# Optimization experiments

Measured on AMD Instinct MI355X. Metric: run time of the kernel, lower is better.

The kernel has to match this reference:

```python
import jax, jax.numpy as jnp
import numpy as np

GROUPS = [[0, 1, 2, 3, 4], [5, 7, 9], [6, 8, 10], [11, 13, 15], [12, 14, 16]]
G = len(GROUPS)
BN_EPS = 1e-5


def _fc_edges(n):
    r = np.repeat(np.arange(n), n)
    c = np.tile(np.arange(n), n)
    m = r != c
    return jnp.asarray(r[m]), jnp.asarray(c[m])


ROW, COL = _fc_edges(G)  # [E], E = G*(G-1) = 20


def _bn(x, scale, bias, mean, var):
    # inference-mode batchnorm over last dim
    return (x - mean) * (scale * jax.lax.rsqrt(var + BN_EPS)) + bias


def setup_inputs() -> dict:
    key = jax.random.key(0)
    ks = jax.random.split(key, 12)
    B, K, C, Ci = 4096, 17, 256, 64
    inp = {
        "x_bk_c": jax.random.normal(ks[0], (B * K, C), jnp.float32),
        "W_down": jax.random.normal(ks[1], (C, Ci), jnp.float32) * 0.05,
        "b_down": jax.random.normal(ks[2], (Ci,), jnp.float32) * 0.05,
        "bn1_scale": jax.random.uniform(ks[3], (Ci,), jnp.float32, 0.5, 1.5),
        "bn1_bias": jax.random.normal(ks[4], (Ci,), jnp.float32) * 0.1,
        "bn1_mean": jax.random.normal(ks[5], (Ci,), jnp.float32) * 0.1,
        "bn1_var": jax.random.uniform(ks[6], (Ci,), jnp.float32, 0.5, 1.5),
        "W_conv": jax.random.normal(ks[7], (Ci, 2 * Ci), jnp.float32) * 0.05,  # 1x1 conv, bias=False
        "bn2_scale": jax.random.uniform(ks[8], (Ci,), jnp.float32, 0.5, 1.5),
        "bn2_bias": jax.random.normal(ks[9], (Ci,), jnp.float32) * 0.1,
        "bn2_mean": jax.random.normal(ks[10], (Ci,), jnp.float32) * 0.1,
        "bn2_var": jax.random.uniform(ks[11], (Ci,), jnp.float32, 0.5, 1.5),
        "W_agg": jax.random.normal(jax.random.fold_in(key, 100), (Ci, C), jnp.float32) * 0.05,
        "b_agg": jax.random.normal(jax.random.fold_in(key, 101), (C,), jnp.float32) * 0.05,
        "B": B,
        "K": K,
    }
    return inp


def reference(x_bk_c, W_down, b_down, bn1_scale, bn1_bias, bn1_mean, bn1_var,
              W_conv, bn2_scale, bn2_bias, bn2_mean, bn2_var, W_agg, b_agg, B, K):
    C = x_bk_c.shape[-1]
    # down-projection + BN + SiLU
    xd = jax.nn.silu(_bn(x_bk_c @ W_down + b_down, bn1_scale, bn1_bias, bn1_mean, bn1_var))
    xd = xd.reshape(B, K, -1)  # [B, K, Ci]
    # per-group mean pooling (static small loop over 5 groups)
    means = jnp.stack([xd[:, g, :].mean(axis=1) for g in GROUPS], axis=1)  # [B, G, Ci]
    # EdgeConv over fully-connected group graph
    x_i = means[:, ROW, :]                                   # [B, E, Ci]
    x_j = means[:, COL, :]
    ef = jnp.concatenate([x_i, x_j - x_i], axis=-1)          # [B, E, 2Ci]
    pe = jax.nn.silu(_bn(ef @ W_conv.T, bn2_scale, bn2_bias, bn2_mean, bn2_var))  # [B, E, Ci]
    agg = jnp.zeros_like(means).at[:, ROW, :].add(pe)        # scatter-add over target nodes
    # per-group attention scores in C_in
    att = jax.nn.sigmoid(agg @ W_agg + b_agg)                # [B, G, C]
    # average group scores over each keypoint's memberships
    M = np.zeros((K, G), np.float32)
    for gi, g in enumerate(GROUPS):
        for kp in g:
            M[kp, gi] += 1.0
    Mj = jnp.asarray(M)
    cnt = Mj.sum(axis=1, keepdims=True)                      # [K, 1]
    ssum = jnp.einsum('kg,bgc->bkc', Mj, att)                # [B, K, C]
    safe = jnp.where(cnt > 0, cnt, 1.0)
    final = jnp.where(cnt > 0, ssum / safe, 1.0)             # ungrouped kps -> 1.0
    return (x_bk_c.reshape(B, K, C) * final).reshape(B * K, C)
```

## Files before the change

kernel.cpp:

```cpp
#include <hip/hip_runtime.h>

typedef float  v4f    __attribute__((ext_vector_type(4)));
typedef float  f32x4  __attribute__((ext_vector_type(4)));
typedef short  bf16x8 __attribute__((ext_vector_type(8)));
typedef short  bf16x4 __attribute__((ext_vector_type(4)));

namespace {
constexpr int XBSTR = 264;
constexpr int XDT   = 24;
constexpr int MWC   = 129;
constexpr int ATS   = 260;
constexpr int MSTR  = 72;
constexpr int FRAG_SLOTS = 5120;

__device__ __forceinline__ float fsilu(float v){ return v/(1.f+__expf(-v)); }
__device__ __forceinline__ float fsigm(float v){ return 1.f/(1.f+__expf(-v)); }

__device__ __forceinline__ unsigned f2bf2(float a, float b){
  unsigned r;
  asm("v_cvt_pk_bf16_f32 %0, %1, %2" : "=v"(r) : "v"(a), "v"(b));
  return r;
}
__device__ __forceinline__ short f2bf(float f){
  unsigned u = __builtin_bit_cast(unsigned, f);
  return (short)((u + 0x7FFFu + ((u>>16)&1u)) >> 16);
}
__device__ __forceinline__ float bf2f(short s){
  unsigned u = ((unsigned)(unsigned short)s) << 16;
  return __builtin_bit_cast(float, u);
}

template<bool USE_WS>
__device__ __forceinline__ bf16x8 get_bd(const bf16x8* wsf, const float* Wd,
                                         int nt, int ks, int l){
  if constexpr (USE_WS) return wsf[(nt*8 + ks)*64 + l];
  bf16x8 f;
  #pragma unroll
  for (int j = 0; j < 8; ++j) f[j] = f2bf(Wd[(ks*32 + (l>>4)*8 + j)*64 + nt*16 + (l&15)]);
  return f;
}
template<bool USE_WS>
__device__ __forceinline__ bf16x8 get_bc(const bf16x8* wsf, const float* Wc,
                                         int nt, int ks, int l){
  if constexpr (USE_WS) return wsf[2048 + (nt*2 + ks)*64 + l];
  const int col = nt*16 + (l&15), cw = col>>6, co = col&63;
  bf16x8 f;
  #pragma unroll
  for (int j = 0; j < 8; ++j) f[j] = f2bf(Wc[co*128 + cw*64 + ks*32 + (l>>4)*8 + j]);
  return f;
}
template<bool USE_WS>
__device__ __forceinline__ bf16x8 get_ba(const bf16x8* wsf, const float* Wa,
                                         int nt, int ks, int l){
  if constexpr (USE_WS) return wsf[3072 + (nt*2 + ks)*64 + l];
  const int col = nt*16 + (l&15);
  bf16x8 f;
  #pragma unroll
  for (int j = 0; j < 8; ++j) f[j] = f2bf(Wa[(ks*32 + (l>>4)*8 + j)*256 + col]);
  return f;
}
}

__global__ __launch_bounds__(256)
void pack_frags(const float* __restrict__ Wd, const float* __restrict__ Wc,
                const float* __restrict__ Wa, bf16x8* __restrict__ wsf)
{
  const int e  = blockIdx.x*256 + threadIdx.x;
  const int l  = e & 63;
  const int fi = e >> 6;
  bf16x8 f;
  if (fi < 32) {
    const int nt = fi >> 3, ks = fi & 7;
    #pragma unroll
    for (int j = 0; j < 8; ++j) f[j] = f2bf(Wd[(ks*32 + (l>>4)*8 + j)*64 + nt*16 + (l&15)]);
  } else if (fi < 48) {
    const int idx = fi - 32, nt = idx >> 1, ks = idx & 1;
    const int col = nt*16 + (l&15), cw = col>>6, co = col&63;
    #pragma unroll
    for (int j = 0; j < 8; ++j) f[j] = f2bf(Wc[co*128 + cw*64 + ks*32 + (l>>4)*8 + j]);
  } else {
    const int idx = fi - 48, nt = idx >> 1, ks = idx & 1;
    const int col = nt*16 + (l&15);
    #pragma unroll
    for (int j = 0; j < 8; ++j) f[j] = f2bf(Wa[(ks*32 + (l>>4)*8 + j)*256 + col]);
  }
  wsf[e] = f;
}

template<bool USE_WS>
__global__ __launch_bounds__(256, 5)
void fused_gnn_v12(const float* __restrict__ x,
                   const float* __restrict__ Wd, const float* __restrict__ bd,
                   const float* __restrict__ bn1s, const float* __restrict__ bn1b,
                   const float* __restrict__ bn1m, const float* __restrict__ bn1v,
                   const float* __restrict__ Wc,
                   const float* __restrict__ bn2s, const float* __restrict__ bn2b,
                   const float* __restrict__ bn2m, const float* __restrict__ bn2v,
                   const float* __restrict__ Wa, const float* __restrict__ ba,
                   const bf16x8* __restrict__ wsf,
                   float* __restrict__ out)
{
  __shared__ short xbf[18*XBSTR];
  __shared__ __align__(16) char uni_raw[3072];
  __shared__ float mw[5*MWC];
  __shared__ short mbf[16*MSTR];
  __shared__ short abf[16*MSTR];

  short* xdT = (short*)uni_raw;
  short* att = (short*)uni_raw;

  const int tid  = threadIdx.x;
  const int l    = tid & 63;
  const int wv   = tid >> 6;
  const int arow = l & 15;
  const int ak8  = (l >> 4) * 8;
  const int b    = blockIdx.x;
  const int colA = wv*16 + arow;

  const float a1r = bn1s[colA] * rsqrtf(bn1v[colA] + 1e-5f);
  const float b1r = (bd[colA] - bn1m[colA])*a1r + bn1b[colA];
  const float a2r = bn2s[l] * rsqrtf(bn2v[l] + 1e-5f);
  const float b2r = bn2b[l] - bn2m[l]*a2r;

  const int c4 = l*4;
  const int r0 = tid >> 6;
  v4f xr0, xr1, xr2, xr3, xr4;
  {
    const v4f* x4 = (const v4f*)(x + (size_t)b * 4352);
    xr0 = x4[tid];        xr1 = x4[256 + tid];
    xr2 = x4[512 + tid];  xr3 = x4[768 + tid];
    if (tid < 64) xr4 = x4[1024 + tid];
    auto store4 = [&](v4f v, int r){
      uint2 u; u.x = f2bf2(v.x, v.y); u.y = f2bf2(v.z, v.w);
      *(uint2*)&xbf[r*XBSTR + c4] = u;
    };
    store4(xr0, r0);      store4(xr1, r0 + 4);
    store4(xr2, r0 + 8);  store4(xr3, r0 + 12);
    if (tid < 64) store4(xr4, 16);
  }
  __syncthreads();

  {
    f32x4 acc0 = {0.f,0.f,0.f,0.f};
    f32x4 acc1 = {0.f,0.f,0.f,0.f};
    const int rowT = (arow == 0) ? 16 : 17;
    #pragma unroll
    for (int h = 0; h < 2; ++h) {
      bf16x8 Bd[4];
      #pragma unroll
      for (int k4 = 0; k4 < 4; ++k4) Bd[k4] = get_bd<USE_WS>(wsf, Wd, wv, h*4 + k4, l);
      #pragma unroll
      for (int k4 = 0; k4 < 4; ++k4) {
        const int ks = h*4 + k4;
        bf16x8 a0 = *(const bf16x8*)&xbf[arow*XBSTR + ks*32 + ak8];
        acc0 = __builtin_amdgcn_mfma_f32_16x16x32_bf16(a0, Bd[k4], acc0, 0, 0, 0);
        bf16x8 a1 = *(const bf16x8*)&xbf[rowT*XBSTR + ks*32 + ak8];
        acc1 = __builtin_amdgcn_mfma_f32_16x16x32_bf16(a1, Bd[k4], acc1, 0, 0, 0);
      }
    }
    const float s0 = fsilu(acc0[0]*a1r + b1r);
    const float s1 = fsilu(acc0[1]*a1r + b1r);
    const float s2 = fsilu(acc0[2]*a1r + b1r);
    const float s3 = fsilu(acc0[3]*a1r + b1r);
    uint2 u; u.x = f2bf2(s0, s1); u.y = f2bf2(s2, s3);
    *(uint2*)&xdT[colA*XDT + (l>>4)*4] = u;
    if ((l >> 4) == 0)
      xdT[colA*XDT + 16] = f2bf(fsilu(acc1[0]*a1r + b1r));
  }
  __syncthreads();

  bf16x8 BcT[2][2];
  #pragma unroll
  for (int t = 0; t < 2; ++t)
    #pragma unroll
    for (int ks = 0; ks < 2; ++ks)
      BcT[t][ks] = get_bc<USE_WS>(wsf, Wc, wv*2 + t, ks, l);

  {
    const int i = l;
    #define XDV(r) bf2f(xdT[i*XDT + (r)])
    if (wv == 0) {
      mbf[0*MSTR + i] = f2bf((XDV(0)+XDV(1)+XDV(2)+XDV(3)+XDV(4))*0.2f);
      mbf[4*MSTR + i] = f2bf((XDV(12)+XDV(14)+XDV(16))*(1.f/3.f));
    } else if (wv == 1) {
      mbf[1*MSTR + i] = f2bf((XDV(5)+XDV(7)+XDV(9))*(1.f/3.f));
    } else if (wv == 2) {
      mbf[2*MSTR + i] = f2bf((XDV(6)+XDV(8)+XDV(10))*(1.f/3.f));
    } else {
      mbf[3*MSTR + i] = f2bf((XDV(11)+XDV(13)+XDV(15))*(1.f/3.f));
    }
    #undef XDV
  }
  __syncthreads();

  {
    bf16x8 am[2];
    #pragma unroll
    for (int ks = 0; ks < 2; ++ks)
      am[ks] = *(const bf16x8*)&mbf[arow*MSTR + ks*32 + ak8];
    #pragma unroll
    for (int t = 0; t < 2; ++t) {
      const int nt = wv*2 + t;
      f32x4 acc = {0.f,0.f,0.f,0.f};
      #pragma unroll
      for (int ks = 0; ks < 2; ++ks)
        acc = __builtin_amdgcn_mfma_f32_16x16x32_bf16(am[ks], BcT[t][ks], acc, 0, 0, 0);
      if ((l >> 4) == 0) {
        #pragma unroll
        for (int j = 0; j < 4; ++j) mw[j*MWC + nt*16 + arow] = acc[j];
      } else if ((l >> 4) == 1) {
        mw[4*MWC + nt*16 + arow] = acc[0];
      }
    }
  }
  __syncthreads();

  bf16x8 BaT[4][2];
  #pragma unroll
  for (int t = 0; t < 4; ++t)
    #pragma unroll
    for (int ks = 0; ks < 2; ++ks)
      BaT[t][ks] = get_ba<USE_WS>(wsf, Wa, wv*4 + t, ks, l);

  {
    const int o = l;
    float m2c[5];
    #pragma unroll
    for (int cc = 0; cc < 5; ++cc) m2c[cc] = mw[cc*MWC + 64 + o];
    auto doG = [&](int g){
      const float bse = mw[g*MWC + o] - m2c[g];
      float s = 0.f;
      #pragma unroll
      for (int cc = 0; cc < 5; ++cc) {
        if (cc != g) s += fsilu((bse + m2c[cc])*a2r + b2r);
      }
      abf[g*MSTR + o] = f2bf(s);
    };
    if (wv == 0) { doG(0); doG(4); }
    else if (wv == 1) doG(1);
    else if (wv == 2) doG(2);
    else doG(3);
  }
  __syncthreads();

  {
    bf16x8 ae[2];
    #pragma unroll
    for (int ks = 0; ks < 2; ++ks)
      ae[ks] = *(const bf16x8*)&abf[arow*MSTR + ks*32 + ak8];
    #pragma unroll
    for (int t = 0; t < 4; ++t) {
      const int nt = wv*4 + t;
      const int colE = nt*16 + arow;
      f32x4 acc = {0.f,0.f,0.f,0.f};
      #pragma unroll
      for (int ks = 0; ks < 2; ++ks)
        acc = __builtin_amdgcn_mfma_f32_16x16x32_bf16(ae[ks], BaT[t][ks], acc, 0, 0, 0);
      const float bav = ba[colE];
      const int q4 = l >> 4;
      if (q4 == 0) {
        #pragma unroll
        for (int j = 0; j < 4; ++j)
          att[j*ATS + colE] = f2bf(fsigm(acc[j] + bav));
      } else if (q4 == 1) {
        att[4*ATS + colE] = f2bf(fsigm(acc[0] + bav));
      }
    }
  }
  __syncthreads();

  {
    float* og = out + (size_t)b*4352;
    constexpr int GOF[17] = {0,0,0,0,0,1,2,1,2,1,2,3,4,3,4,3,4};
    auto emit = [&](v4f xv, int k){
      const bf16x4 a4 = *(const bf16x4*)&att[GOF[k]*ATS + c4];
      v4f o;
      o.x = xv.x * bf2f(a4[0]);
      o.y = xv.y * bf2f(a4[1]);
      o.z = xv.z * bf2f(a4[2]);
      o.w = xv.w * bf2f(a4[3]);
      *(v4f*)&og[k*256 + c4] = o;
    };
    emit(xr0, r0);      emit(xr1, r0 + 4);
    emit(xr2, r0 + 8);  emit(xr3, r0 + 12);
    if (tid < 64) emit(xr4, 16);
  }
}

extern "C" void kernel_launch(void* const* d_in, const int* in_sizes, int n_in,
                              void* d_out, int out_size, void* d_ws, size_t ws_size,
                              hipStream_t stream) {
    (void)n_in; (void)out_size;
    const float* x   = (const float*)d_in[0];
    const float* Wd  = (const float*)d_in[1];
    const float* bd  = (const float*)d_in[2];
    const float* s1  = (const float*)d_in[3];
    const float* b1  = (const float*)d_in[4];
    const float* m1  = (const float*)d_in[5];
    const float* v1  = (const float*)d_in[6];
    const float* Wc  = (const float*)d_in[7];
    const float* s2  = (const float*)d_in[8];
    const float* b2  = (const float*)d_in[9];
    const float* m2  = (const float*)d_in[10];
    const float* v2  = (const float*)d_in[11];
    const float* Wa  = (const float*)d_in[12];
    const float* ba  = (const float*)d_in[13];

    const int Btot = in_sizes[0] / (17 * 256);
    bf16x8* wsf = (bf16x8*)d_ws;

    if (ws_size >= (size_t)FRAG_SLOTS * 16) {
        pack_frags<<<FRAG_SLOTS/256, 256, 0, stream>>>(Wd, Wc, Wa, wsf);
        fused_gnn_v12<true><<<Btot, 256, 0, stream>>>(
            x, Wd, bd, s1, b1, m1, v1, Wc, s2, b2, m2, v2, Wa, ba,
            wsf, (float*)d_out);
    } else {
        fused_gnn_v12<false><<<Btot, 256, 0, stream>>>(
            x, Wd, bd, s1, b1, m1, v1, Wc, s2, b2, m2, v2, Wa, ba,
            wsf, (float*)d_out);
    }
}
```

Baseline: 41.52 us.

## Process two batch items per block with prefetched second input tile

```diff
diff --git a/kernel.cpp b/kernel.cpp
--- a/kernel.cpp
+++ b/kernel.cpp
@@ -88,8 +88,8 @@
 }
 
 template<bool USE_WS>
-__global__ __launch_bounds__(256, 5)
-void fused_gnn_v12(const float* __restrict__ x,
+__global__ __launch_bounds__(256, 7)
+void fused_gnn_v13(const float* __restrict__ x,
                    const float* __restrict__ Wd, const float* __restrict__ bd,
                    const float* __restrict__ bn1s, const float* __restrict__ bn1b,
                    const float* __restrict__ bn1m, const float* __restrict__ bn1v,
@@ -114,176 +114,193 @@
   const int wv   = tid >> 6;
   const int arow = l & 15;
   const int ak8  = (l >> 4) * 8;
-  const int b    = blockIdx.x;
+  const int b0   = blockIdx.x * 2;
   const int colA = wv*16 + arow;
+  const int c4   = l*4;
+  const int r0   = tid >> 6;
 
   const float a1r = bn1s[colA] * rsqrtf(bn1v[colA] + 1e-5f);
   const float b1r = (bd[colA] - bn1m[colA])*a1r + bn1b[colA];
   const float a2r = bn2s[l] * rsqrtf(bn2v[l] + 1e-5f);
   const float b2r = bn2b[l] - bn2m[l]*a2r;
 
-  const int c4 = l*4;
-  const int r0 = tid >> 6;
-  v4f xr0, xr1, xr2, xr3, xr4;
+  auto store4 = [&](v4f v, int r){
+    uint2 u; u.x = f2bf2(v.x, v.y); u.y = f2bf2(v.z, v.w);
+    *(uint2*)&xbf[r*XBSTR + c4] = u;
+  };
+
+  v4f xr[2][5];
   {
-    const v4f* x4 = (const v4f*)(x + (size_t)b * 4352);
-    xr0 = x4[tid];        xr1 = x4[256 + tid];
-    xr2 = x4[512 + tid];  xr3 = x4[768 + tid];
-    if (tid < 64) xr4 = x4[1024 + tid];
-    auto store4 = [&](v4f v, int r){
-      uint2 u; u.x = f2bf2(v.x, v.y); u.y = f2bf2(v.z, v.w);
-      *(uint2*)&xbf[r*XBSTR + c4] = u;
-    };
-    store4(xr0, r0);      store4(xr1, r0 + 4);
-    store4(xr2, r0 + 8);  store4(xr3, r0 + 12);
-    if (tid < 64) store4(xr4, 16);
+    const v4f* x4 = (const v4f*)(x + (size_t)b0 * 4352);
+    #pragma unroll
+    for (int i = 0; i < 4; ++i) xr[0][i] = x4[i*256 + tid];
+    if (tid < 64) xr[0][4] = x4[1024 + tid];
+    store4(xr[0][0], r0);      store4(xr[0][1], r0 + 4);
+    store4(xr[0][2], r0 + 8);  store4(xr[0][3], r0 + 12);
+    if (tid < 64) store4(xr[0][4], 16);
+    const v4f* y4 = x4 + 1088;
+    #pragma unroll
+    for (int i = 0; i < 4; ++i) xr[1][i] = y4[i*256 + tid];
+    if (tid < 64) xr[1][4] = y4[1024 + tid];
   }
   __syncthreads();
 
-  {
-    f32x4 acc0 = {0.f,0.f,0.f,0.f};
-    f32x4 acc1 = {0.f,0.f,0.f,0.f};
-    const int rowT = (arow == 0) ? 16 : 17;
-    #pragma unroll
-    for (int h = 0; h < 2; ++h) {
-      bf16x8 Bd[4];
-      #pragma unroll
-      for (int k4 = 0; k4 < 4; ++k4) Bd[k4] = get_bd<USE_WS>(wsf, Wd, wv, h*4 + k4, l);
-      #pragma unroll
-      for (int k4 = 0; k4 < 4; ++k4) {
-        const int ks = h*4 + k4;
-        bf16x8 a0 = *(const bf16x8*)&xbf[arow*XBSTR + ks*32 + ak8];
-        acc0 = __builtin_amdgcn_mfma_f32_16x16x32_bf16(a0, Bd[k4], acc0, 0, 0, 0);
-        bf16x8 a1 = *(const bf16x8*)&xbf[rowT*XBSTR + ks*32 + ak8];
-        acc1 = __builtin_amdgcn_mfma_f32_16x16x32_bf16(a1, Bd[k4], acc1, 0, 0, 0);
+  #pragma unroll
+  for (int it = 0; it < 2; ++it) {
+    const int b = b0 + it;
+
+    {
+      f32x4 acc0 = {0.f,0.f,0.f,0.f};
+      f32x4 acc1 = {0.f,0.f,0.f,0.f};
+      const int rowT = (arow == 0) ? 16 : 17;
+      #pragma unroll
+      for (int h = 0; h < 2; ++h) {
+        bf16x8 Bd[4];
+        #pragma unroll
+        for (int k4 = 0; k4 < 4; ++k4) Bd[k4] = get_bd<USE_WS>(wsf, Wd, wv, h*4 + k4, l);
+        #pragma unroll
+        for (int k4 = 0; k4 < 4; ++k4) {
+          const int ks = h*4 + k4;
+          bf16x8 a0 = *(const bf16x8*)&xbf[arow*XBSTR + ks*32 + ak8];
+          acc0 = __builtin_amdgcn_mfma_f32_16x16x32_bf16(a0, Bd[k4], acc0, 0, 0, 0);
+          bf16x8 a1 = *(const bf16x8*)&xbf[rowT*XBSTR + ks*32 + ak8];
+          acc1 = __builtin_amdgcn_mfma_f32_16x16x32_bf16(a1, Bd[k4], acc1, 0, 0, 0);
+        }
       }
-    }
-    const float s0 = fsilu(acc0[0]*a1r + b1r);
-    const float s1 = fsilu(acc0[1]*a1r + b1r);
-    const float s2 = fsilu(acc0[2]*a1r + b1r);
-    const float s3 = fsilu(acc0[3]*a1r + b1r);
-    uint2 u; u.x = f2bf2(s0, s1); u.y = f2bf2(s2, s3);
-    *(uint2*)&xdT[colA*XDT + (l>>4)*4] = u;
-    if ((l >> 4) == 0)
-      xdT[colA*XDT + 16] = f2bf(fsilu(acc1[0]*a1r + b1r));
-  }
-  __syncthreads();
-
-  bf16x8 BcT[2][2];
-  #pragma unroll
-  for (int t = 0; t < 2; ++t)
-    #pragma unroll
-    for (int ks = 0; ks < 2; ++ks)
-      BcT[t][ks] = get_bc<USE_WS>(wsf, Wc, wv*2 + t, ks, l);
-
-  {
-    const int i = l;
-    #define XDV(r) bf2f(xdT[i*XDT + (r)])
-    if (wv == 0) {
-      mbf[0*MSTR + i] = f2bf((XDV(0)+XDV(1)+XDV(2)+XDV(3)+XDV(4))*0.2f);
-      mbf[4*MSTR + i] = f2bf((XDV(12)+XDV(14)+XDV(16))*(1.f/3.f));
-    } else if (wv == 1) {
-      mbf[1*MSTR + i] = f2bf((XDV(5)+XDV(7)+XDV(9))*(1.f/3.f));
-    } else if (wv == 2) {
-      mbf[2*MSTR + i] = f2bf((XDV(6)+XDV(8)+XDV(10))*(1.f/3.f));
-    } else {
-      mbf[3*MSTR + i] = f2bf((XDV(11)+XDV(13)+XDV(15))*(1.f/3.f));
-    }
-    #undef XDV
-  }
-  __syncthreads();
-
-  {
-    bf16x8 am[2];
-    #pragma unroll
-    for (int ks = 0; ks < 2; ++ks)
-      am[ks] = *(const bf16x8*)&mbf[arow*MSTR + ks*32 + ak8];
-    #pragma unroll
-    for (int t = 0; t < 2; ++t) {
-      const int nt = wv*2 + t;
-      f32x4 acc = {0.f,0.f,0.f,0.f};
+      const float s0 = fsilu(acc0[0]*a1r + b1r);
+      const float s1 = fsilu(acc0[1]*a1r + b1r);
+      const float s2 = fsilu(acc0[2]*a1r + b1r);
+      const float s3 = fsilu(acc0[3]*a1r + b1r);
+      uint2 u; u.x = f2bf2(s0, s1); u.y = f2bf2(s2, s3);
+      *(uint2*)&xdT[colA*XDT + (l>>4)*4] = u;
+      if ((l >> 4) == 0)
+        xdT[colA*XDT + 16] = f2bf(fsilu(acc1[0]*a1r + b1r));
+    }
+    __syncthreads();
+
+    if (it == 0) {
+      store4(xr[1][0], r0);      store4(xr[1][1], r0 + 4);
+      store4(xr[1][2], r0 + 8);  store4(xr[1][3], r0 + 12);
+      if (tid < 64) store4(xr[1][4], 16);
+    }
+
+    bf16x8 BcT[2][2];
+    #pragma unroll
+    for (int t = 0; t < 2; ++t)
       #pragma unroll
       for (int ks = 0; ks < 2; ++ks)
-        acc = __builtin_amdgcn_mfma_f32_16x16x32_bf16(am[ks], BcT[t][ks], acc, 0, 0, 0);
-      if ((l >> 4) == 0) {
-        #pragma unroll
-        for (int j = 0; j < 4; ++j) mw[j*MWC + nt*16 + arow] = acc[j];
-      } else if ((l >> 4) == 1) {
-        mw[4*MWC + nt*16 + arow] = acc[0];
+        BcT[t][ks] = get_bc<USE_WS>(wsf, Wc, wv*2 + t, ks, l);
+
+    {
+      const int i = l;
+      #define XDV(r) bf2f(xdT[i*XDT + (r)])
+      if (wv == 0) {
+        mbf[0*MSTR + i] = f2bf((XDV(0)+XDV(1)+XDV(2)+XDV(3)+XDV(4))*0.2f);
+        mbf[4*MSTR + i] = f2bf((XDV(12)+XDV(14)+XDV(16))*(1.f/3.f));
+      } else if (wv == 1) {
+        mbf[1*MSTR + i] = f2bf((XDV(5)+XDV(7)+XDV(9))*(1.f/3.f));
+      } else if (wv == 2) {
+        mbf[2*MSTR + i] = f2bf((XDV(6)+XDV(8)+XDV(10))*(1.f/3.f));
+      } else {
+        mbf[3*MSTR + i] = f2bf((XDV(11)+XDV(13)+XDV(15))*(1.f/3.f));
       }
-    }
-  }
-  __syncthreads();
-
-  bf16x8 BaT[4][2];
-  #pragma unroll
-  for (int t = 0; t < 4; ++t)
-    #pragma unroll
-    for (int ks = 0; ks < 2; ++ks)
-      BaT[t][ks] = get_ba<USE_WS>(wsf, Wa, wv*4 + t, ks, l);
-
-  {
-    const int o = l;
-    float m2c[5];
-    #pragma unroll
-    for (int cc = 0; cc < 5; ++cc) m2c[cc] = mw[cc*MWC + 64 + o];
-    auto doG = [&](int g){
-      const float bse = mw[g*MWC + o] - m2c[g];
-      float s = 0.f;
-      #pragma unroll
-      for (int cc = 0; cc < 5; ++cc) {
-        if (cc != g) s += fsilu((bse + m2c[cc])*a2r + b2r);
+      #undef XDV
+    }
+    __syncthreads();
+
+    {
+      bf16x8 am[2];
+      #pragma unroll
+      for (int ks = 0; ks < 2; ++ks)
+        am[ks] = *(const bf16x8*)&mbf[arow*MSTR + ks*32 + ak8];
+      #pragma unroll
+      for (int t = 0; t < 2; ++t) {
+        const int nt = wv*2 + t;
+        f32x4 acc = {0.f,0.f,0.f,0.f};
+        #pragma unroll
+        for (int ks = 0; ks < 2; ++ks)
+          acc = __builtin_amdgcn_mfma_f32_16x16x32_bf16(am[ks], BcT[t][ks], acc, 0, 0, 0);
+        if ((l >> 4) == 0) {
+          #pragma unroll
+          for (int j = 0; j < 4; ++j) mw[j*MWC + nt*16 + arow] = acc[j];
+        } else if ((l >> 4) == 1) {
+          mw[4*MWC + nt*16 + arow] = acc[0];
+        }
       }
-      abf[g*MSTR + o] = f2bf(s);
-    };
-    if (wv == 0) { doG(0); doG(4); }
-    else if (wv == 1) doG(1);
-    else if (wv == 2) doG(2);
-    else doG(3);
-  }
-  __syncthreads();
-
-  {
-    bf16x8 ae[2];
-    #pragma unroll
-    for (int ks = 0; ks < 2; ++ks)
-      ae[ks] = *(const bf16x8*)&abf[arow*MSTR + ks*32 + ak8];
-    #pragma unroll
-    for (int t = 0; t < 4; ++t) {
-      const int nt = wv*4 + t;
-      const int colE = nt*16 + arow;
-      f32x4 acc = {0.f,0.f,0.f,0.f};
+    }
+    __syncthreads();
+
+    bf16x8 BaT[4][2];
+    #pragma unroll
+    for (int t = 0; t < 4; ++t)
       #pragma unroll
       for (int ks = 0; ks < 2; ++ks)
-        acc = __builtin_amdgcn_mfma_f32_16x16x32_bf16(ae[ks], BaT[t][ks], acc, 0, 0, 0);
-      const float bav = ba[colE];
-      const int q4 = l >> 4;
-      if (q4 == 0) {
-        #pragma unroll
-        for (int j = 0; j < 4; ++j)
-          att[j*ATS + colE] = f2bf(fsigm(acc[j] + bav));
-      } else if (q4 == 1) {
-        att[4*ATS + colE] = f2bf(fsigm(acc[0] + bav));
+        BaT[t][ks] = get_ba<USE_WS>(wsf, Wa, wv*4 + t, ks, l);
+
+    {
+      const int o = l;
+      float m2c[5];
+      #pragma unroll
+      for (int cc = 0; cc < 5; ++cc) m2c[cc] = mw[cc*MWC + 64 + o];
+      auto doG = [&](int g){
+        const float bse = mw[g*MWC + o] - m2c[g];
+        float s = 0.f;
+        #pragma unroll
+        for (int cc = 0; cc < 5; ++cc) {
+          if (cc != g) s += fsilu((bse + m2c[cc])*a2r + b2r);
+        }
+        abf[g*MSTR + o] = f2bf(s);
+      };
+      if (wv == 0) { doG(0); doG(4); }
+      else if (wv == 1) doG(1);
+      else if (wv == 2) doG(2);
+      else doG(3);
+    }
+    __syncthreads();
+
+    {
+      bf16x8 ae[2];
+      #pragma unroll
+      for (int ks = 0; ks < 2; ++ks)
+        ae[ks] = *(const bf16x8*)&abf[arow*MSTR + ks*32 + ak8];
+      #pragma unroll
+      for (int t = 0; t < 4; ++t) {
+        const int nt = wv*4 + t;
+        const int colE = nt*16 + arow;
+        f32x4 acc = {0.f,0.f,0.f,0.f};
+        #pragma unroll
+        for (int ks = 0; ks < 2; ++ks)
+          acc = __builtin_amdgcn_mfma_f32_16x16x32_bf16(ae[ks], BaT[t][ks], acc, 0, 0, 0);
+        const float bav = ba[colE];
+        const int q4 = l >> 4;
+        if (q4 == 0) {
+          #pragma unroll
+          for (int j = 0; j < 4; ++j)
+            att[j*ATS + colE] = f2bf(fsigm(acc[j] + bav));
+        } else if (q4 == 1) {
+          att[4*ATS + colE] = f2bf(fsigm(acc[0] + bav));
+        }
       }
     }
-  }
-  __syncthreads();
-
-  {
-    float* og = out + (size_t)b*4352;
-    constexpr int GOF[17] = {0,0,0,0,0,1,2,1,2,1,2,3,4,3,4,3,4};
-    auto emit = [&](v4f xv, int k){
-      const bf16x4 a4 = *(const bf16x4*)&att[GOF[k]*ATS + c4];
-      v4f o;
-      o.x = xv.x * bf2f(a4[0]);
-      o.y = xv.y * bf2f(a4[1]);
-      o.z = xv.z * bf2f(a4[2]);
-      o.w = xv.w * bf2f(a4[3]);
-      *(v4f*)&og[k*256 + c4] = o;
-    };
-    emit(xr0, r0);      emit(xr1, r0 + 4);
-    emit(xr2, r0 + 8);  emit(xr3, r0 + 12);
-    if (tid < 64) emit(xr4, 16);
+    __syncthreads();
+
+    {
+      float* og = out + (size_t)b*4352;
+      constexpr int GOF[17] = {0,0,0,0,0,1,2,1,2,1,2,3,4,3,4,3,4};
+      auto emit = [&](v4f xv, int k){
+        const bf16x4 a4 = *(const bf16x4*)&att[GOF[k]*ATS + c4];
+        v4f o;
+        o.x = xv.x * bf2f(a4[0]);
+        o.y = xv.y * bf2f(a4[1]);
+        o.z = xv.z * bf2f(a4[2]);
+        o.w = xv.w * bf2f(a4[3]);
+        *(v4f*)&og[k*256 + c4] = o;
+      };
+      emit(xr[it][0], r0);      emit(xr[it][1], r0 + 4);
+      emit(xr[it][2], r0 + 8);  emit(xr[it][3], r0 + 12);
+      if (tid < 64) emit(xr[it][4], 16);
+    }
+    if (it == 0) __syncthreads();
   }
 }
 
@@ -307,15 +324,16 @@
     const float* ba  = (const float*)d_in[13];
 
     const int Btot = in_sizes[0] / (17 * 256);
+    const int GRID = Btot / 2;
     bf16x8* wsf = (bf16x8*)d_ws;
 
     if (ws_size >= (size_t)FRAG_SLOTS * 16) {
         pack_frags<<<FRAG_SLOTS/256, 256, 0, stream>>>(Wd, Wc, Wa, wsf);
-        fused_gnn_v12<true><<<Btot, 256, 0, stream>>>(
+        fused_gnn_v13<true><<<GRID, 256, 0, stream>>>(
             x, Wd, bd, s1, b1, m1, v1, Wc, s2, b2, m2, v2, Wa, ba,
             wsf, (float*)d_out);
     } else {
-        fused_gnn_v12<false><<<Btot, 256, 0, stream>>>(
+        fused_gnn_v13<false><<<GRID, 256, 0, stream>>>(
             x, Wd, bd, s1, b1, m1, v1, Wc, s2, b2, m2, v2, Wa, ba,
             wsf, (float*)d_out);
     }
```

Result: slower. 139.7 us (+236.5%).

## Process two batch items per block and prefetch the second item's input

Applied to the files above, without the earlier changes.

```diff
diff --git a/kernel.cpp b/kernel.cpp
--- a/kernel.cpp
+++ b/kernel.cpp
@@ -89,7 +89,7 @@
 
 template<bool USE_WS>
 __global__ __launch_bounds__(256, 5)
-void fused_gnn_v12(const float* __restrict__ x,
+void fused_gnn_v14(const float* __restrict__ x,
                    const float* __restrict__ Wd, const float* __restrict__ bd,
                    const float* __restrict__ bn1s, const float* __restrict__ bn1b,
                    const float* __restrict__ bn1m, const float* __restrict__ bn1v,
@@ -114,48 +114,39 @@
   const int wv   = tid >> 6;
   const int arow = l & 15;
   const int ak8  = (l >> 4) * 8;
-  const int b    = blockIdx.x;
+  const int b0   = blockIdx.x * 2;
   const int colA = wv*16 + arow;
+  const int c4   = l*4;
+  const int r0   = tid >> 6;
 
   const float a1r = bn1s[colA] * rsqrtf(bn1v[colA] + 1e-5f);
   const float b1r = (bd[colA] - bn1m[colA])*a1r + bn1b[colA];
   const float a2r = bn2s[l] * rsqrtf(bn2v[l] + 1e-5f);
   const float b2r = bn2b[l] - bn2m[l]*a2r;
 
-  const int c4 = l*4;
-  const int r0 = tid >> 6;
-  v4f xr0, xr1, xr2, xr3, xr4;
-  {
-    const v4f* x4 = (const v4f*)(x + (size_t)b * 4352);
-    xr0 = x4[tid];        xr1 = x4[256 + tid];
-    xr2 = x4[512 + tid];  xr3 = x4[768 + tid];
-    if (tid < 64) xr4 = x4[1024 + tid];
-    auto store4 = [&](v4f v, int r){
-      uint2 u; u.x = f2bf2(v.x, v.y); u.y = f2bf2(v.z, v.w);
-      *(uint2*)&xbf[r*XBSTR + c4] = u;
-    };
-    store4(xr0, r0);      store4(xr1, r0 + 4);
-    store4(xr2, r0 + 8);  store4(xr3, r0 + 12);
-    if (tid < 64) store4(xr4, 16);
-  }
-  __syncthreads();
-
-  {
+  auto store4 = [&](v4f v, int r){
+    uint2 u; u.x = f2bf2(v.x, v.y); u.y = f2bf2(v.z, v.w);
+    *(uint2*)&xbf[r*XBSTR + c4] = u;
+  };
+
+  auto phaseA = [&](){
     f32x4 acc0 = {0.f,0.f,0.f,0.f};
     f32x4 acc1 = {0.f,0.f,0.f,0.f};
     const int rowT = (arow == 0) ? 16 : 17;
     #pragma unroll
     for (int h = 0; h < 2; ++h) {
-      bf16x8 Bd[4];
-      #pragma unroll
-      for (int k4 = 0; k4 < 4; ++k4) Bd[k4] = get_bd<USE_WS>(wsf, Wd, wv, h*4 + k4, l);
+      bf16x8 Bd0 = get_bd<USE_WS>(wsf, Wd, wv, h*4 + 0, l);
+      bf16x8 Bd1 = get_bd<USE_WS>(wsf, Wd, wv, h*4 + 1, l);
+      bf16x8 Bd2 = get_bd<USE_WS>(wsf, Wd, wv, h*4 + 2, l);
+      bf16x8 Bd3 = get_bd<USE_WS>(wsf, Wd, wv, h*4 + 3, l);
       #pragma unroll
       for (int k4 = 0; k4 < 4; ++k4) {
         const int ks = h*4 + k4;
+        const bf16x8 Bd = (k4==0)?Bd0:(k4==1)?Bd1:(k4==2)?Bd2:Bd3;
         bf16x8 a0 = *(const bf16x8*)&xbf[arow*XBSTR + ks*32 + ak8];
-        acc0 = __builtin_amdgcn_mfma_f32_16x16x32_bf16(a0, Bd[k4], acc0, 0, 0, 0);
+        acc0 = __builtin_amdgcn_mfma_f32_16x16x32_bf16(a0, Bd, acc0, 0, 0, 0);
         bf16x8 a1 = *(const bf16x8*)&xbf[rowT*XBSTR + ks*32 + ak8];
-        acc1 = __builtin_amdgcn_mfma_f32_16x16x32_bf16(a1, Bd[k4], acc1, 0, 0, 0);
+        acc1 = __builtin_amdgcn_mfma_f32_16x16x32_bf16(a1, Bd, acc1, 0, 0, 0);
       }
     }
     const float s0 = fsilu(acc0[0]*a1r + b1r);
@@ -166,17 +157,9 @@
     *(uint2*)&xdT[colA*XDT + (l>>4)*4] = u;
     if ((l >> 4) == 0)
       xdT[colA*XDT + 16] = f2bf(fsilu(acc1[0]*a1r + b1r));
-  }
-  __syncthreads();
-
-  bf16x8 BcT[2][2];
-  #pragma unroll
-  for (int t = 0; t < 2; ++t)
-    #pragma unroll
-    for (int ks = 0; ks < 2; ++ks)
-      BcT[t][ks] = get_bc<USE_WS>(wsf, Wc, wv*2 + t, ks, l);
-
-  {
+  };
+
+  auto phaseB1 = [&](){
     const int i = l;
     #define XDV(r) bf2f(xdT[i*XDT + (r)])
     if (wv == 0) {
@@ -190,21 +173,17 @@
       mbf[3*MSTR + i] = f2bf((XDV(11)+XDV(13)+XDV(15))*(1.f/3.f));
     }
     #undef XDV
-  }
-  __syncthreads();
-
-  {
-    bf16x8 am[2];
-    #pragma unroll
-    for (int ks = 0; ks < 2; ++ks)
-      am[ks] = *(const bf16x8*)&mbf[arow*MSTR + ks*32 + ak8];
+  };
+
+  auto phaseB2 = [&](){
+    bf16x8 am0 = *(const bf16x8*)&mbf[arow*MSTR + 0*32 + ak8];
+    bf16x8 am1 = *(const bf16x8*)&mbf[arow*MSTR + 1*32 + ak8];
     #pragma unroll
     for (int t = 0; t < 2; ++t) {
       const int nt = wv*2 + t;
       f32x4 acc = {0.f,0.f,0.f,0.f};
-      #pragma unroll
-      for (int ks = 0; ks < 2; ++ks)
-        acc = __builtin_amdgcn_mfma_f32_16x16x32_bf16(am[ks], BcT[t][ks], acc, 0, 0, 0);
+      acc = __builtin_amdgcn_mfma_f32_16x16x32_bf16(am0, get_bc<USE_WS>(wsf, Wc, nt, 0, l), acc, 0, 0, 0);
+      acc = __builtin_amdgcn_mfma_f32_16x16x32_bf16(am1, get_bc<USE_WS>(wsf, Wc, nt, 1, l), acc, 0, 0, 0);
       if ((l >> 4) == 0) {
         #pragma unroll
         for (int j = 0; j < 4; ++j) mw[j*MWC + nt*16 + arow] = acc[j];
@@ -212,50 +191,39 @@
         mw[4*MWC + nt*16 + arow] = acc[0];
       }
     }
-  }
-  __syncthreads();
-
-  bf16x8 BaT[4][2];
-  #pragma unroll
-  for (int t = 0; t < 4; ++t)
-    #pragma unroll
-    for (int ks = 0; ks < 2; ++ks)
-      BaT[t][ks] = get_ba<USE_WS>(wsf, Wa, wv*4 + t, ks, l);
-
-  {
+  };
+
+  auto phaseB3 = [&](){
     const int o = l;
-    float m2c[5];
-    #pragma unroll
-    for (int cc = 0; cc < 5; ++cc) m2c[cc] = mw[cc*MWC + 64 + o];
-    auto doG = [&](int g){
-      const float bse = mw[g*MWC + o] - m2c[g];
+    float m2c0 = mw[0*MWC + 64 + o], m2c1 = mw[1*MWC + 64 + o];
+    float m2c2 = mw[2*MWC + 64 + o], m2c3 = mw[3*MWC + 64 + o];
+    float m2c4 = mw[4*MWC + 64 + o];
+    auto doG = [&](int g, float m2g){
+      const float bse = mw[g*MWC + o] - m2g;
       float s = 0.f;
-      #pragma unroll
-      for (int cc = 0; cc < 5; ++cc) {
-        if (cc != g) s += fsilu((bse + m2c[cc])*a2r + b2r);
-      }
+      if (g != 0) s += fsilu((bse + m2c0)*a2r + b2r);
+      if (g != 1) s += fsilu((bse + m2c1)*a2r + b2r);
+      if (g != 2) s += fsilu((bse + m2c2)*a2r + b2r);
+      if (g != 3) s += fsilu((bse + m2c3)*a2r + b2r);
+      if (g != 4) s += fsilu((bse + m2c4)*a2r + b2r);
       abf[g*MSTR + o] = f2bf(s);
     };
-    if (wv == 0) { doG(0); doG(4); }
-    else if (wv == 1) doG(1);
-    else if (wv == 2) doG(2);
-    else doG(3);
-  }
-  __syncthreads();
-
-  {
-    bf16x8 ae[2];
-    #pragma unroll
-    for (int ks = 0; ks < 2; ++ks)
-      ae[ks] = *(const bf16x8*)&abf[arow*MSTR + ks*32 + ak8];
+    if (wv == 0) { doG(0, m2c0); doG(4, m2c4); }
+    else if (wv == 1) doG(1, m2c1);
+    else if (wv == 2) doG(2, m2c2);
+    else doG(3, m2c3);
+  };
+
+  auto phaseE = [&](){
+    bf16x8 ae0 = *(const bf16x8*)&abf[arow*MSTR + 0*32 + ak8];
+    bf16x8 ae1 = *(const bf16x8*)&abf[arow*MSTR + 1*32 + ak8];
     #pragma unroll
     for (int t = 0; t < 4; ++t) {
       const int nt = wv*4 + t;
       const int colE = nt*16 + arow;
       f32x4 acc = {0.f,0.f,0.f,0.f};
-      #pragma unroll
-      for (int ks = 0; ks < 2; ++ks)
-        acc = __builtin_amdgcn_mfma_f32_16x16x32_bf16(ae[ks], BaT[t][ks], acc, 0, 0, 0);
+      acc = __builtin_amdgcn_mfma_f32_16x16x32_bf16(ae0, get_ba<USE_WS>(wsf, Wa, nt, 0, l), acc, 0, 0, 0);
+      acc = __builtin_amdgcn_mfma_f32_16x16x32_bf16(ae1, get_ba<USE_WS>(wsf, Wa, nt, 1, l), acc, 0, 0, 0);
       const float bav = ba[colE];
       const int q4 = l >> 4;
       if (q4 == 0) {
@@ -266,10 +234,9 @@
         att[4*ATS + colE] = f2bf(fsigm(acc[0] + bav));
       }
     }
-  }
-  __syncthreads();
-
-  {
+  };
+
+  auto phaseF = [&](v4f f0, v4f f1, v4f f2, v4f f3, v4f f4, int b){
     float* og = out + (size_t)b*4352;
     constexpr int GOF[17] = {0,0,0,0,0,1,2,1,2,1,2,3,4,3,4,3,4};
     auto emit = [&](v4f xv, int k){
@@ -281,10 +248,59 @@
       o.w = xv.w * bf2f(a4[3]);
       *(v4f*)&og[k*256 + c4] = o;
     };
-    emit(xr0, r0);      emit(xr1, r0 + 4);
-    emit(xr2, r0 + 8);  emit(xr3, r0 + 12);
-    if (tid < 64) emit(xr4, 16);
+    emit(f0, r0);      emit(f1, r0 + 4);
+    emit(f2, r0 + 8);  emit(f3, r0 + 12);
+    if (tid < 64) emit(f4, 16);
+  };
+
+  v4f a0, a1, a2, a3, a4;
+  {
+    const v4f* x4 = (const v4f*)(x + (size_t)b0 * 4352);
+    a0 = x4[tid];        a1 = x4[256 + tid];
+    a2 = x4[512 + tid];  a3 = x4[768 + tid];
+    if (tid < 64) a4 = x4[1024 + tid];
+    store4(a0, r0);      store4(a1, r0 + 4);
+    store4(a2, r0 + 8);  store4(a3, r0 + 12);
+    if (tid < 64) store4(a4, 16);
   }
+  __syncthreads();
+
+  phaseA();
+  __syncthreads();
+
+  v4f c0, c1, c2, c3, c4r;
+  {
+    const v4f* y4 = (const v4f*)(x + (size_t)(b0+1) * 4352);
+    c0 = y4[tid];        c1 = y4[256 + tid];
+    c2 = y4[512 + tid];  c3 = y4[768 + tid];
+    if (tid < 64) c4r = y4[1024 + tid];
+  }
+
+  phaseB1();
+  __syncthreads();
+  phaseB2();
+  __syncthreads();
+  phaseB3();
+  __syncthreads();
+  phaseE();
+  __syncthreads();
+  phaseF(a0, a1, a2, a3, a4, b0);
+  store4(c0, r0);      store4(c1, r0 + 4);
+  store4(c2, r0 + 8);  store4(c3, r0 + 12);
+  if (tid < 64) store4(c4r, 16);
+  __syncthreads();
+
+  phaseA();
+  __syncthreads();
+  phaseB1();
+  __syncthreads();
+  phaseB2();
+  __syncthreads();
+  phaseB3();
+  __syncthreads();
+  phaseE();
+  __syncthreads();
+  phaseF(c0, c1, c2, c3, c4r, b0 + 1);
 }
 
 extern "C" void kernel_launch(void* const* d_in, const int* in_sizes, int n_in,
@@ -307,15 +323,16 @@
     const float* ba  = (const float*)d_in[13];
 
     const int Btot = in_sizes[0] / (17 * 256);
+    const int GRID = Btot / 2;
     bf16x8* wsf = (bf16x8*)d_ws;
 
     if (ws_size >= (size_t)FRAG_SLOTS * 16) {
         pack_frags<<<FRAG_SLOTS/256, 256, 0, stream>>>(Wd, Wc, Wa, wsf);
-        fused_gnn_v12<true><<<Btot, 256, 0, stream>>>(
+        fused_gnn_v14<true><<<GRID, 256, 0, stream>>>(
             x, Wd, bd, s1, b1, m1, v1, Wc, s2, b2, m2, v2, Wa, ba,
             wsf, (float*)d_out);
     } else {
-        fused_gnn_v12<false><<<Btot, 256, 0, stream>>>(
+        fused_gnn_v14<false><<<GRID, 256, 0, stream>>>(
             x, Wd, bd, s1, b1, m1, v1, Wc, s2, b2, m2, v2, Wa, ba,
             wsf, (float*)d_out);
     }
```

New measurement: 87.56 us. 2.11x slower.

## Process four batches per block and re-read x from bf16 LDS for output

Applied to the files above, without the earlier changes.

```diff
diff --git a/kernel.cpp b/kernel.cpp
--- a/kernel.cpp
+++ b/kernel.cpp
@@ -11,6 +11,7 @@
 constexpr int MWC   = 129;
 constexpr int ATS   = 260;
 constexpr int MSTR  = 72;
+constexpr int NB    = 4;
 constexpr int FRAG_SLOTS = 5120;
 
 __device__ __forceinline__ float fsilu(float v){ return v/(1.f+__expf(-v)); }
@@ -88,8 +89,8 @@
 }
 
 template<bool USE_WS>
-__global__ __launch_bounds__(256, 5)
-void fused_gnn_v12(const float* __restrict__ x,
+__global__ __launch_bounds__(256, 6)
+void fused_gnn_v15(const float* __restrict__ x,
                    const float* __restrict__ Wd, const float* __restrict__ bd,
                    const float* __restrict__ bn1s, const float* __restrict__ bn1b,
                    const float* __restrict__ bn1m, const float* __restrict__ bn1v,
@@ -114,176 +115,182 @@
   const int wv   = tid >> 6;
   const int arow = l & 15;
   const int ak8  = (l >> 4) * 8;
-  const int b    = blockIdx.x;
   const int colA = wv*16 + arow;
+  const int c4   = l*4;
+  const int r0   = tid >> 6;
 
   const float a1r = bn1s[colA] * rsqrtf(bn1v[colA] + 1e-5f);
   const float b1r = (bd[colA] - bn1m[colA])*a1r + bn1b[colA];
   const float a2r = bn2s[l] * rsqrtf(bn2v[l] + 1e-5f);
   const float b2r = bn2b[l] - bn2m[l]*a2r;
 
-  const int c4 = l*4;
-  const int r0 = tid >> 6;
-  v4f xr0, xr1, xr2, xr3, xr4;
-  {
-    const v4f* x4 = (const v4f*)(x + (size_t)b * 4352);
-    xr0 = x4[tid];        xr1 = x4[256 + tid];
-    xr2 = x4[512 + tid];  xr3 = x4[768 + tid];
-    if (tid < 64) xr4 = x4[1024 + tid];
-    auto store4 = [&](v4f v, int r){
-      uint2 u; u.x = f2bf2(v.x, v.y); u.y = f2bf2(v.z, v.w);
-      *(uint2*)&xbf[r*XBSTR + c4] = u;
-    };
-    store4(xr0, r0);      store4(xr1, r0 + 4);
-    store4(xr2, r0 + 8);  store4(xr3, r0 + 12);
-    if (tid < 64) store4(xr4, 16);
-  }
-  __syncthreads();
-
-  {
-    f32x4 acc0 = {0.f,0.f,0.f,0.f};
-    f32x4 acc1 = {0.f,0.f,0.f,0.f};
-    const int rowT = (arow == 0) ? 16 : 17;
-    #pragma unroll
-    for (int h = 0; h < 2; ++h) {
-      bf16x8 Bd[4];
-      #pragma unroll
-      for (int k4 = 0; k4 < 4; ++k4) Bd[k4] = get_bd<USE_WS>(wsf, Wd, wv, h*4 + k4, l);
-      #pragma unroll
-      for (int k4 = 0; k4 < 4; ++k4) {
-        const int ks = h*4 + k4;
-        bf16x8 a0 = *(const bf16x8*)&xbf[arow*XBSTR + ks*32 + ak8];
-        acc0 = __builtin_amdgcn_mfma_f32_16x16x32_bf16(a0, Bd[k4], acc0, 0, 0, 0);
-        bf16x8 a1 = *(const bf16x8*)&xbf[rowT*XBSTR + ks*32 + ak8];
-        acc1 = __builtin_amdgcn_mfma_f32_16x16x32_bf16(a1, Bd[k4], acc1, 0, 0, 0);
-      }
-    }
-    const float s0 = fsilu(acc0[0]*a1r + b1r);
-    const float s1 = fsilu(acc0[1]*a1r + b1r);
-    const float s2 = fsilu(acc0[2]*a1r + b1r);
-    const float s3 = fsilu(acc0[3]*a1r + b1r);
-    uint2 u; u.x = f2bf2(s0, s1); u.y = f2bf2(s2, s3);
-    *(uint2*)&xdT[colA*XDT + (l>>4)*4] = u;
-    if ((l >> 4) == 0)
-      xdT[colA*XDT + 16] = f2bf(fsilu(acc1[0]*a1r + b1r));
-  }
-  __syncthreads();
-
-  bf16x8 BcT[2][2];
-  #pragma unroll
-  for (int t = 0; t < 2; ++t)
-    #pragma unroll
-    for (int ks = 0; ks < 2; ++ks)
-      BcT[t][ks] = get_bc<USE_WS>(wsf, Wc, wv*2 + t, ks, l);
-
-  {
-    const int i = l;
-    #define XDV(r) bf2f(xdT[i*XDT + (r)])
-    if (wv == 0) {
-      mbf[0*MSTR + i] = f2bf((XDV(0)+XDV(1)+XDV(2)+XDV(3)+XDV(4))*0.2f);
-      mbf[4*MSTR + i] = f2bf((XDV(12)+XDV(14)+XDV(16))*(1.f/3.f));
-    } else if (wv == 1) {
-      mbf[1*MSTR + i] = f2bf((XDV(5)+XDV(7)+XDV(9))*(1.f/3.f));
-    } else if (wv == 2) {
-      mbf[2*MSTR + i] = f2bf((XDV(6)+XDV(8)+XDV(10))*(1.f/3.f));
-    } else {
-      mbf[3*MSTR + i] = f2bf((XDV(11)+XDV(13)+XDV(15))*(1.f/3.f));
-    }
-    #undef XDV
-  }
-  __syncthreads();
-
-  {
-    bf16x8 am[2];
-    #pragma unroll
-    for (int ks = 0; ks < 2; ++ks)
-      am[ks] = *(const bf16x8*)&mbf[arow*MSTR + ks*32 + ak8];
-    #pragma unroll
-    for (int t = 0; t < 2; ++t) {
-      const int nt = wv*2 + t;
-      f32x4 acc = {0.f,0.f,0.f,0.f};
+  for (int it = 0; it < NB; ++it) {
+    const int b = blockIdx.x * NB + it;
+
+    {
+      const v4f* x4 = (const v4f*)(x + (size_t)b * 4352);
+      auto ldst = [&](int slot, int r){
+        const v4f v = x4[slot*256 + tid];
+        uint2 u; u.x = f2bf2(v.x, v.y); u.y = f2bf2(v.z, v.w);
+        *(uint2*)&xbf[r*XBSTR + c4] = u;
+      };
+      ldst(0, r0);      ldst(1, r0 + 4);
+      ldst(2, r0 + 8);  ldst(3, r0 + 12);
+      if (tid < 64) {
+        const v4f v = x4[1024 + tid];
+        uint2 u; u.x = f2bf2(v.x, v.y); u.y = f2bf2(v.z, v.w);
+        *(uint2*)&xbf[16*XBSTR + c4] = u;
+      }
+    }
+    __syncthreads();
+
+    {
+      f32x4 acc0 = {0.f,0.f,0.f,0.f};
+      f32x4 acc1 = {0.f,0.f,0.f,0.f};
+      const int rowT = (arow == 0) ? 16 : 17;
+      #pragma unroll
+      for (int h = 0; h < 2; ++h) {
+        bf16x8 Bd[4];
+        #pragma unroll
+        for (int k4 = 0; k4 < 4; ++k4) Bd[k4] = get_bd<USE_WS>(wsf, Wd, wv, h*4 + k4, l);
+        #pragma unroll
+        for (int k4 = 0; k4 < 4; ++k4) {
+          const int ks = h*4 + k4;
+          bf16x8 a0 = *(const bf16x8*)&xbf[arow*XBSTR + ks*32 + ak8];
+          acc0 = __builtin_amdgcn_mfma_f32_16x16x32_bf16(a0, Bd[k4], acc0, 0, 0, 0);
+          bf16x8 a1 = *(const bf16x8*)&xbf[rowT*XBSTR + ks*32 + ak8];
+          acc1 = __builtin_amdgcn_mfma_f32_16x16x32_bf16(a1, Bd[k4], acc1, 0, 0, 0);
+        }
+      }
+      const float s0 = fsilu(acc0[0]*a1r + b1r);
+      const float s1 = fsilu(acc0[1]*a1r + b1r);
+      const float s2 = fsilu(acc0[2]*a1r + b1r);
+      const float s3 = fsilu(acc0[3]*a1r + b1r);
+      uint2 u; u.x = f2bf2(s0, s1); u.y = f2bf2(s2, s3);
+      *(uint2*)&xdT[colA*XDT + (l>>4)*4] = u;
+      if ((l >> 4) == 0)
+        xdT[colA*XDT + 16] = f2bf(fsilu(acc1[0]*a1r + b1r));
+    }
+    __syncthreads();
+
+    bf16x8 BcT[2][2];
+    #pragma unroll
+    for (int t = 0; t < 2; ++t)
       #pragma unroll
       for (int ks = 0; ks < 2; ++ks)
-        acc = __builtin_amdgcn_mfma_f32_16x16x32_bf16(am[ks], BcT[t][ks], acc, 0, 0, 0);
-      if ((l >> 4) == 0) {
-        #pragma unroll
-        for (int j = 0; j < 4; ++j) mw[j*MWC + nt*16 + arow] = acc[j];
-      } else if ((l >> 4) == 1) {
-        mw[4*MWC + nt*16 + arow] = acc[0];
-      }
-    }
-  }
-  __syncthreads();
-
-  bf16x8 BaT[4][2];
-  #pragma unroll
-  for (int t = 0; t < 4; ++t)
-    #pragma unroll
-    for (int ks = 0; ks < 2; ++ks)
-      BaT[t][ks] = get_ba<USE_WS>(wsf, Wa, wv*4 + t, ks, l);
-
-  {
-    const int o = l;
-    float m2c[5];
-    #pragma unroll
-    for (int cc = 0; cc < 5; ++cc) m2c[cc] = mw[cc*MWC + 64 + o];
-    auto doG = [&](int g){
-      const float bse = mw[g*MWC + o] - m2c[g];
-      float s = 0.f;
-      #pragma unroll
-      for (int cc = 0; cc < 5; ++cc) {
-        if (cc != g) s += fsilu((bse + m2c[cc])*a2r + b2r);
-      }
-      abf[g*MSTR + o] = f2bf(s);
-    };
-    if (wv == 0) { doG(0); doG(4); }
-    else if (wv == 1) doG(1);
-    else if (wv == 2) doG(2);
-    else doG(3);
-  }
-  __syncthreads();
-
-  {
-    bf16x8 ae[2];
-    #pragma unroll
-    for (int ks = 0; ks < 2; ++ks)
-      ae[ks] = *(const bf16x8*)&abf[arow*MSTR + ks*32 + ak8];
-    #pragma unroll
-    for (int t = 0; t < 4; ++t) {
-      const int nt = wv*4 + t;
-      const int colE = nt*16 + arow;
-      f32x4 acc = {0.f,0.f,0.f,0.f};
+        BcT[t][ks] = get_bc<USE_WS>(wsf, Wc, wv*2 + t, ks, l);
+
+    {
+      const int i = l;
+      #define XDV(r) bf2f(xdT[i*XDT + (r)])
+      if (wv == 0) {
+        mbf[0*MSTR + i] = f2bf((XDV(0)+XDV(1)+XDV(2)+XDV(3)+XDV(4))*0.2f);
+        mbf[4*MSTR + i] = f2bf((XDV(12)+XDV(14)+XDV(16))*(1.f/3.f));
+      } else if (wv == 1) {
+        mbf[1*MSTR + i] = f2bf((XDV(5)+XDV(7)+XDV(9))*(1.f/3.f));
+      } else if (wv == 2) {
+        mbf[2*MSTR + i] = f2bf((XDV(6)+XDV(8)+XDV(10))*(1.f/3.f));
+      } else {
+        mbf[3*MSTR + i] = f2bf((XDV(11)+XDV(13)+XDV(15))*(1.f/3.f));
+      }
+      #undef XDV
+    }
+    __syncthreads();
+
+    {
+      bf16x8 am[2];
       #pragma unroll
       for (int ks = 0; ks < 2; ++ks)
-        acc = __builtin_amdgcn_mfma_f32_16x16x32_bf16(ae[ks], BaT[t][ks], acc, 0, 0, 0);
-      const float bav = ba[colE];
-      const int q4 = l >> 4;
-      if (q4 == 0) {
-        #pragma unroll
-        for (int j = 0; j < 4; ++j)
-          att[j*ATS + colE] = f2bf(fsigm(acc[j] + bav));
-      } else if (q4 == 1) {
-        att[4*ATS + colE] = f2bf(fsigm(acc[0] + bav));
-      }
-    }
-  }
-  __syncthreads();
-
-  {
-    float* og = out + (size_t)b*4352;
-    constexpr int GOF[17] = {0,0,0,0,0,1,2,1,2,1,2,3,4,3,4,3,4};
-    auto emit = [&](v4f xv, int k){
-      const bf16x4 a4 = *(const bf16x4*)&att[GOF[k]*ATS + c4];
-      v4f o;
-      o.x = xv.x * bf2f(a4[0]);
-      o.y = xv.y * bf2f(a4[1]);
-      o.z = xv.z * bf2f(a4[2]);
-      o.w = xv.w * bf2f(a4[3]);
-      *(v4f*)&og[k*256 + c4] = o;
-    };
-    emit(xr0, r0);      emit(xr1, r0 + 4);
-    emit(xr2, r0 + 8);  emit(xr3, r0 + 12);
-    if (tid < 64) emit(xr4, 16);
+        am[ks] = *(const bf16x8*)&mbf[arow*MSTR + ks*32 + ak8];
+      #pragma unroll
+      for (int t = 0; t < 2; ++t) {
+        const int nt = wv*2 + t;
+        f32x4 acc = {0.f,0.f,0.f,0.f};
+        #pragma unroll
+        for (int ks = 0; ks < 2; ++ks)
+          acc = __builtin_amdgcn_mfma_f32_16x16x32_bf16(am[ks], BcT[t][ks], acc, 0, 0, 0);
+        if ((l >> 4) == 0) {
+          #pragma unroll
+          for (int j = 0; j < 4; ++j) mw[j*MWC + nt*16 + arow] = acc[j];
+        } else if ((l >> 4) == 1) {
+          mw[4*MWC + nt*16 + arow] = acc[0];
+        }
+      }
+    }
+    __syncthreads();
+
+    bf16x8 BaT[4][2];
+    #pragma unroll
+    for (int t = 0; t < 4; ++t)
+      #pragma unroll
+      for (int ks = 0; ks < 2; ++ks)
+        BaT[t][ks] = get_ba<USE_WS>(wsf, Wa, wv*4 + t, ks, l);
+
+    {
+      const int o = l;
+      float m2c[5];
+      #pragma unroll
+      for (int cc = 0; cc < 5; ++cc) m2c[cc] = mw[cc*MWC + 64 + o];
+      auto doG = [&](int g){
+        const float bse = mw[g*MWC + o] - m2c[g];
+        float s = 0.f;
+        #pragma unroll
+        for (int cc = 0; cc < 5; ++cc) {
+          if (cc != g) s += fsilu((bse + m2c[cc])*a2r + b2r);
+        }
+        abf[g*MSTR + o] = f2bf(s);
+      };
+      if (wv == 0) { doG(0); doG(4); }
+      else if (wv == 1) doG(1);
+      else if (wv == 2) doG(2);
+      else doG(3);
+    }
+    __syncthreads();
+
+    {
+      bf16x8 ae[2];
+      #pragma unroll
+      for (int ks = 0; ks < 2; ++ks)
+        ae[ks] = *(const bf16x8*)&abf[arow*MSTR + ks*32 + ak8];
+      #pragma unroll
+      for (int t = 0; t < 4; ++t) {
+        const int nt = wv*4 + t;
+        const int colE = nt*16 + arow;
+        f32x4 acc = {0.f,0.f,0.f,0.f};
+        #pragma unroll
+        for (int ks = 0; ks < 2; ++ks)
+          acc = __builtin_amdgcn_mfma_f32_16x16x32_bf16(ae[ks], BaT[t][ks], acc, 0, 0, 0);
+        const float bav = ba[colE];
+        const int q4 = l >> 4;
+        if (q4 == 0) {
+          #pragma unroll
+          for (int j = 0; j < 4; ++j)
+            att[j*ATS + colE] = f2bf(fsigm(acc[j] + bav));
+        } else if (q4 == 1) {
+          att[4*ATS + colE] = f2bf(fsigm(acc[0] + bav));
+        }
+      }
+    }
+    __syncthreads();
+
+    {
+      float* og = out + (size_t)b*4352;
+      constexpr int GOF[17] = {0,0,0,0,0,1,2,1,2,1,2,3,4,3,4,3,4};
+      auto emit = [&](int k){
+        const bf16x4 xv4 = *(const bf16x4*)&xbf[k*XBSTR + c4];
+        const bf16x4 a4  = *(const bf16x4*)&att[GOF[k]*ATS + c4];
+        v4f o;
+        o.x = bf2f(xv4[0]) * bf2f(a4[0]);
+        o.y = bf2f(xv4[1]) * bf2f(a4[1]);
+        o.z = bf2f(xv4[2]) * bf2f(a4[2]);
+        o.w = bf2f(xv4[3]) * bf2f(a4[3]);
+        *(v4f*)&og[k*256 + c4] = o;
+      };
+      emit(r0);      emit(r0 + 4);
+      emit(r0 + 8);  emit(r0 + 12);
+      if (tid < 64) emit(16);
+    }
+    __syncthreads();
   }
 }
 
@@ -307,15 +314,16 @@
     const float* ba  = (const float*)d_in[13];
 
     const int Btot = in_sizes[0] / (17 * 256);
+    const int GRID = Btot / NB;
     bf16x8* wsf = (bf16x8*)d_ws;
 
     if (ws_size >= (size_t)FRAG_SLOTS * 16) {
         pack_frags<<<FRAG_SLOTS/256, 256, 0, stream>>>(Wd, Wc, Wa, wsf);
-        fused_gnn_v12<true><<<Btot, 256, 0, stream>>>(
+        fused_gnn_v15<true><<<GRID, 256, 0, stream>>>(
             x, Wd, bd, s1, b1, m1, v1, Wc, s2, b2, m2, v2, Wa, ba,
             wsf, (float*)d_out);
     } else {
-        fused_gnn_v12<false><<<Btot, 256, 0, stream>>>(
+        fused_gnn_v15<false><<<GRID, 256, 0, stream>>>(
             x, Wd, bd, s1, b1, m1, v1, Wc, s2, b2, m2, v2, Wa, ba,
             wsf, (float*)d_out);
     }
```

After: 74.12 us. +78.5%, slower.
